# Kernel optimization log

Measured on AMD Instinct MI355X. Metric: run time of the kernel, lower is better.

Reference implementation:

```python
import jax, jax.numpy as jnp
import numpy as np

B, C, N, INPUT_DIM = 16, 19, 64, 200
VQ_DIM = 64
NUM_EMBED = 8192
FREQ = INPUT_DIM // 2 + 1  # 101 rfft bins


def setup_inputs() -> dict:
    key = jax.random.key(0)
    k_x, k_pa, k_pp, k_ca, k_cp = jax.random.split(key, 5)
    x = jax.random.normal(k_x, (B, C, N, INPUT_DIM), dtype=jnp.float32)
    # xavier_normal for [FREQ, VQ_DIM]
    std = float(np.sqrt(2.0 / (FREQ + VQ_DIM)))
    proj_amp = jax.random.normal(k_pa, (FREQ, VQ_DIM), dtype=jnp.float32) * std
    proj_phase = jax.random.normal(k_pp, (FREQ, VQ_DIM), dtype=jnp.float32) * std
    codebook_amp = jax.random.uniform(k_ca, (NUM_EMBED, VQ_DIM), dtype=jnp.float32)
    codebook_phase = jax.random.uniform(k_cp, (NUM_EMBED, VQ_DIM), dtype=jnp.float32)
    return {"x": x, "proj_amp": proj_amp, "proj_phase": proj_phase,
            "codebook_amp": codebook_amp, "codebook_phase": codebook_phase}


def _l2norm(v):
    return v / jnp.linalg.norm(v, axis=-1, keepdims=True)


def reference(x, proj_amp, proj_phase, codebook_amp, codebook_phase):
    # rfft over last dim with ortho norm -> [B,C,N,FREQ] complex
    x_fft = jnp.fft.rfft(x, axis=-1, norm="ortho")
    amp = jnp.abs(x_fft)
    phase = jnp.angle(x_fft)
    # project to vq space and L2-normalize features and codebooks
    feat_amp = _l2norm(amp @ proj_amp)        # [B,C,N,D]
    feat_phase = _l2norm(phase @ proj_phase)  # [B,C,N,D]
    cb_amp = _l2norm(codebook_amp)            # [M,D]
    cb_phase = _l2norm(codebook_phase)        # [M,D]
    # cosine similarity vs codebook, argmax over codebook axis
    sim_amp = jnp.einsum("bcnd,md->bcnm", feat_amp, cb_amp)
    sim_phase = jnp.einsum("bcnd,md->bcnm", feat_phase, cb_phase)
    idx_amp = jnp.argmax(sim_amp, axis=-1)
    idx_phase = jnp.argmax(sim_phase, axis=-1)
    return idx_amp, idx_phase
```

## Files before the change

kernel.cpp:

```cpp
#include <hip/hip_runtime.h>
#include <math.h>

constexpr int ROWS  = 19456;
constexpr int IN_DIM = 200;
constexpr int FREQ  = 101;
constexpr int VQD   = 64;
constexpr int NEMB  = 8192;
constexpr int DFT_BLOCKS = ROWS / 8;

typedef __attribute__((ext_vector_type(8))) short short8;
typedef __attribute__((ext_vector_type(4))) float floatx4;

__device__ __forceinline__ unsigned short f2bf(float v) {
    unsigned int u = __builtin_bit_cast(unsigned int, v);
    unsigned int r = u + 0x7fffu + ((u >> 16) & 1u);
    return (unsigned short)(r >> 16);
}
__device__ __forceinline__ float bf2f(unsigned short b) {
    unsigned int u = ((unsigned int)b) << 16;
    return __builtin_bit_cast(float, u);
}

__device__ __forceinline__ void cis_exact(int r, double& c, double& s) {
    if (r == 0)        { c =  1.0; s =  0.0; }
    else if (r == 50)  { c =  0.0; s = -1.0; }
    else if (r == 100) { c = -1.0; s =  0.0; }
    else if (r == 150) { c =  0.0; s =  1.0; }
    else {
        double ang = -6.283185307179586476925286766559 * (double)r / (double)IN_DIM;
        c = cos(ang); s = sin(ang);
    }
}

#define GLOAD_LDS(gp, lp) __builtin_amdgcn_global_load_lds( \
    (const __attribute__((address_space(1))) unsigned int*)(gp), \
    (__attribute__((address_space(3))) unsigned int*)(lp), 16, 0, 0)

constexpr size_t align256(size_t x) { return (x + 255) & ~(size_t)255; }
constexpr size_t SZ_FB    = (size_t)2 * ROWS * VQD * sizeof(unsigned short);
constexpr size_t OFF_FTH  = 0;
constexpr size_t OFF_FTL  = align256(OFF_FTH + SZ_FB);
constexpr size_t SZ_CBB   = (size_t)2 * NEMB * VQD * sizeof(unsigned short);
constexpr size_t OFF_CBH  = align256(OFF_FTL + SZ_FB);
constexpr size_t OFF_CBL  = align256(OFF_CBH + SZ_CBB);
constexpr size_t SZ_FD    = (size_t)2 * ROWS * VQD * sizeof(double);
constexpr size_t OFF_FD   = align256(OFF_CBL + SZ_CBB);
constexpr size_t SZ_INV   = (size_t)2 * NEMB * sizeof(double);
constexpr size_t OFF_INV  = align256(OFF_FD + SZ_FD);
constexpr size_t SZ_PI    = (size_t)2 * 4 * ROWS * sizeof(int);
constexpr size_t OFF_PI1  = align256(OFF_INV + SZ_INV);
constexpr size_t OFF_PI2  = align256(OFF_PI1 + SZ_PI);

__global__ __launch_bounds__(256) void dft_cb_kernel(
    const float* __restrict__ x, const float* __restrict__ projA, const float* __restrict__ projP,
    const float* __restrict__ cbA, const float* __restrict__ cbP,
    unsigned short* __restrict__ ftH, unsigned short* __restrict__ ftL, double* __restrict__ featD,
    unsigned short* __restrict__ cbH, unsigned short* __restrict__ cbL, double* __restrict__ invnD)
{
    __shared__ __align__(16) char smem[32128];
    const int tid = threadIdx.x;

    if (blockIdx.x >= DFT_BLOCKS) {
        float* tile = (float*)smem;
        float* inv  = (float*)(smem + 16640);
        const int bid2 = blockIdx.x - DFT_BLOCKS;
        const int which = bid2 >> 7;
        const int m0 = (bid2 & 127) * 64;
        const float* cb = which ? cbP : cbA;
        for (int e = tid; e < 4096; e += 256) {
            int c = e >> 6, d = e & 63;
            tile[c * 65 + d] = cb[(size_t)(m0 + c) * VQD + d];
        }
        __syncthreads();
        if (tid < 64) {
            double s = 0.0;
            for (int d2 = 0; d2 < 64; ++d2) { double v = (double)tile[tid * 65 + d2]; s += v * v; }
            inv[tid] = (float)(1.0 / sqrt(s));
            invnD[(size_t)which * NEMB + m0 + tid] = 1.0 / sqrt(s);
        }
        __syncthreads();
        for (int e = tid; e < 4096; e += 256) {
            int c = e >> 6, d = e & 63;
            float v = tile[c * 65 + d] * inv[c];
            unsigned short hb = f2bf(v);
            unsigned short lb = f2bf(v - bf2f(hb));
            size_t o = ((size_t)which * NEMB + m0 + c) * VQD + d;
            cbH[o] = hb; cbL[o] = lb;
        }
        return;
    }

    float*  xsT  = (float*)smem;
    double* xpD  = (double*)(smem + 6400);
    double* xmD  = (double*)(smem + 12800);
    double* reS  = (double*)(smem + 19200);
    double* imS  = (double*)(smem + 25664);
    double* reT  = (double*)smem;
    double* imT  = (double*)(smem + 6464);
    double* accS = (double*)smem;
    const int r0 = blockIdx.x * 8;

    for (int e = tid; e < 8 * IN_DIM; e += 256) {
        int r = e / IN_DIM, n = e - r * IN_DIM;
        xsT[n * 8 + r] = x[(size_t)(r0 + r) * IN_DIM + n];
    }
    __syncthreads();

    for (int e = tid; e < 99 * 8; e += 256) {
        int n = (e >> 3) + 1, r = e & 7;
        double a = (double)xsT[n * 8 + r];
        double b = (double)xsT[(IN_DIM - n) * 8 + r];
        xpD[n * 8 + r] = a + b;
        xmD[n * 8 + r] = a - b;
    }
    __syncthreads();

    const int k = tid & 127, half = tid >> 7;
    double re[8], im[8];
    if (k < FREQ) {
        double c1, s1;
        cis_exact(k, c1, s1);
        const int n0 = half ? 51 : 1;
        double wc, ws;
        cis_exact((int)(((long long)k * n0) % IN_DIM), wc, ws);
#pragma unroll
        for (int r = 0; r < 8; ++r) { re[r] = 0.0; im[r] = 0.0; }
        if (half) {
            double sg = (k & 1) ? -1.0 : 1.0;
#pragma unroll
            for (int r = 0; r < 8; ++r)
                re[r] = (double)xsT[r] + sg * (double)xsT[100 * 8 + r];
        }
        const int nEnd = half ? 100 : 51;
        for (int n = n0; n < nEnd; ++n) {
            const double* xpn = xpD + n * 8;
            const double* xmn = xmD + n * 8;
#pragma unroll
            for (int r = 0; r < 8; ++r) {
                re[r] = fma(xpn[r], wc, re[r]);
                im[r] = fma(xmn[r], ws, im[r]);
            }
            double nwc = wc * c1 - ws * s1;
            double nws = wc * s1 + ws * c1;
            wc = nwc; ws = nws;
        }
        if (half) {
#pragma unroll
            for (int r = 0; r < 8; ++r) { reS[k * 8 + r] = re[r]; imS[k * 8 + r] = im[r]; }
        }
    }
    __syncthreads();
    if (half == 0 && k < FREQ) {
#pragma unroll
        for (int r = 0; r < 8; ++r) { re[r] += reS[k * 8 + r]; im[r] += imS[k * 8 + r]; }
#pragma unroll
        for (int r = 0; r < 8; ++r) { reT[k * 8 + r] = re[r]; imT[k * 8 + r] = im[r]; }
    }
    __syncthreads();
    for (int e = tid; e < FREQ * 8; e += 256) {
        double c = reT[e], sn = imT[e];
        reS[e] = sqrt(c * c + sn * sn);
        imS[e] = atan2(sn, c);
    }
    __syncthreads();

    const int d = tid & 63, which = (tid >> 6) & 1, grp = tid >> 7;
    const float*  proj = which ? projP : projA;
    const double* src  = which ? imS : reS;
    double acc[8];
#pragma unroll
    for (int r = 0; r < 8; ++r) acc[r] = 0.0;
    const int kkA = grp ? 51 : 0;
    const int kkB = grp ? FREQ : 51;
    for (int kk = kkA; kk < kkB; ++kk) {
        double p = (double)proj[kk * VQD + d];
#pragma unroll
        for (int r = 0; r < 8; ++r) acc[r] += src[kk * 8 + r] * p;
    }
    if (grp) {
#pragma unroll
        for (int r = 0; r < 8; ++r) accS[(tid & 127) * 8 + r] = acc[r];
    }
    __syncthreads();
    if (grp == 0) {
#pragma unroll
        for (int r = 0; r < 8; ++r) acc[r] += accS[tid * 8 + r];
#pragma unroll
        for (int r = 0; r < 8; ++r) {
            size_t rowi = (size_t)which * ROWS + r0 + r;
            float vf = (float)acc[r];
            unsigned short hb = f2bf(vf);
            unsigned short lb = f2bf(vf - bf2f(hb));
            ftH[rowi * VQD + d] = hb;
            ftL[rowi * VQD + d] = lb;
            featD[rowi * VQD + d] = acc[r];
        }
    }
}

#define MFMA(a, b, c) __builtin_amdgcn_mfma_f32_16x16x32_bf16(a, b, c, 0, 0, 0)
#define UPD(val, s) do { float _v = (val); \
    bool _c1 = _v > b1v[s]; bool _c2 = _v > b2v[s]; \
    b2v[s] = _c1 ? b1v[s] : (_c2 ? _v : b2v[s]); \
    b2i[s] = _c1 ? b1i[s] : (_c2 ? idx : b2i[s]); \
    b1v[s] = _c1 ? _v : b1v[s]; \
    b1i[s] = _c1 ? idx : b1i[s]; } while (0)

__global__ __launch_bounds__(256, 3) void argmax_kernel(
    const unsigned short* __restrict__ ftH, const unsigned short* __restrict__ ftL,
    const unsigned short* __restrict__ cbH, const unsigned short* __restrict__ cbL,
    int* __restrict__ pi1, int* __restrict__ pi2)
{
    __shared__ __align__(16) char lds[33792];
    const int tid = threadIdx.x;
    const int f = blockIdx.y, z = blockIdx.z;
    const int r0 = blockIdx.x * 128;
    const int w = tid >> 6, lane = tid & 63;
    const int q = lane >> 4, cl = lane & 15;

    const unsigned short* ftHb = ftH + (size_t)f * ROWS * VQD;
    const unsigned short* ftLb = ftL + (size_t)f * ROWS * VQD;
    const unsigned short* cbHb = cbH + (size_t)f * NEMB * VQD;
    const unsigned short* cbLb = cbL + (size_t)f * NEMB * VQD;

    short8 aH00, aH01, aH10, aH11, aL00, aL01, aL10, aL11;
    {
        const size_t baseA = (size_t)(r0 + w * 32 + cl) * VQD + q * 8;
        const size_t baseB = baseA + (size_t)16 * VQD;
        aH00 = *(const short8*)(ftHb + baseA);
        aH01 = *(const short8*)(ftHb + baseA + 32);
        aH10 = *(const short8*)(ftHb + baseB);
        aH11 = *(const short8*)(ftHb + baseB + 32);
        aL00 = *(const short8*)(ftLb + baseA);
        aL01 = *(const short8*)(ftLb + baseA + 32);
        aL10 = *(const short8*)(ftLb + baseB);
        aL11 = *(const short8*)(ftLb + baseB + 32);
    }

    float b1v[8], b2v[8]; int b1i[8], b2i[8];
#pragma unroll
    for (int s = 0; s < 8; ++s) { b1v[s] = -INFINITY; b2v[s] = -INFINITY; b1i[s] = 0; b2i[s] = 0; }

    const int cBase = tid >> 3;
    const int jel   = (((tid & 7) ^ (cBase & 7)) << 3);
    const unsigned short* gH = cbHb + (size_t)(z * 2048 + cBase) * VQD + jel;
    const unsigned short* gL = cbLb + (size_t)(z * 2048 + cBase) * VQD + jel;

    const int p0 = ((q ^ (cl & 7)) << 4);
    const int p1 = p0 ^ 64;

#pragma unroll
    for (int r = 0; r < 2; ++r) {
        const size_t gofs = (size_t)(32 * r) * VQD;
        GLOAD_LDS(gH + gofs, lds + w * 1024 + r * 4096);
        GLOAD_LDS(gL + gofs, lds + 8192 + w * 1024 + r * 4096);
    }

    for (int it = 0; it < 32; ++it) {
        __syncthreads();
        if (it < 31) {
            char* nbuf = lds + ((it + 1) & 1) * 16384;
            const size_t gbase = (size_t)((it + 1) * 64) * VQD;
#pragma unroll
            for (int r = 0; r < 2; ++r) {
                const size_t gofs = gbase + (size_t)(32 * r) * VQD;
                GLOAD_LDS(gH + gofs, nbuf + w * 1024 + r * 4096);
                GLOAD_LDS(gL + gofs, nbuf + 8192 + w * 1024 + r * 4096);
            }
        }

        const char* buf = lds + (it & 1) * 16384;
        const int cbase = z * 2048 + it * 64;
#pragma unroll
        for (int nt = 0; nt < 4; ++nt) {
            const char* row = buf + (nt * 16 + cl) * 128;
            short8 bH0 = *(const short8*)(row + p0);
            short8 bH1 = *(const short8*)(row + p1);
            short8 bL0 = *(const short8*)(row + 8192 + p0);
            short8 bL1 = *(const short8*)(row + 8192 + p1);

            floatx4 acc0 = {0.f, 0.f, 0.f, 0.f};
            floatx4 acc1 = {0.f, 0.f, 0.f, 0.f};
            acc0 = MFMA(aH00, bH0, acc0);  acc1 = MFMA(aH10, bH0, acc1);
            acc0 = MFMA(aH01, bH1, acc0);  acc1 = MFMA(aH11, bH1, acc1);
            acc0 = MFMA(aH00, bL0, acc0);  acc1 = MFMA(aH10, bL0, acc1);
            acc0 = MFMA(aH01, bL1, acc0);  acc1 = MFMA(aH11, bL1, acc1);
            acc0 = MFMA(aL00, bH0, acc0);  acc1 = MFMA(aL10, bH0, acc1);
            acc0 = MFMA(aL01, bH1, acc0);  acc1 = MFMA(aL11, bH1, acc1);

            const int idx = cbase + nt * 16 + cl;
#pragma unroll
            for (int i = 0; i < 4; ++i) { UPD(acc0[i], i); UPD(acc1[i], 4 + i); }
        }
    }

    __syncthreads();
    float* redv = (float*)lds;
    int*   redi = (int*)(lds + 128 * 33 * 4);
#pragma unroll
    for (int s = 0; s < 8; ++s) {
        int rowl = w * 32 + ((s & 4) << 2) + q * 4 + (s & 3);
        int base = rowl * 33 + cl * 2;
        redv[base]     = b1v[s]; redi[base]     = b1i[s];
        redv[base + 1] = b2v[s]; redi[base + 1] = b2i[s];
    }
    __syncthreads();
    if (tid < 128) {
        float v1 = -INFINITY, v2 = -INFINITY; int i1 = 0x7fffffff, i2 = 0x7fffffff;
        for (int e = 0; e < 32; ++e) {
            float v = redv[tid * 33 + e]; int id = redi[tid * 33 + e];
            if (v > v1 || (v == v1 && id < i1)) { v2 = v1; i2 = i1; v1 = v; i1 = id; }
            else if (v > v2 || (v == v2 && id < i2)) { v2 = v; i2 = id; }
        }
        size_t p = ((size_t)(f * 4 + z)) * ROWS + r0 + tid;
        pi1[p] = i1; pi2[p] = i2;
    }
}

__global__ __launch_bounds__(256) void rescore_kernel(
    const double* __restrict__ featD, const double* __restrict__ invnD,
    const float* __restrict__ cbA, const float* __restrict__ cbP,
    const int* __restrict__ pi1, const int* __restrict__ pi2,
    int* __restrict__ out)
{
    const int tid = threadIdx.x;
    const int lane = tid & 63, wave = tid >> 6;
    const int task = blockIdx.x * 4 + wave;
    const int f = task / ROWS;
    const int row = task - f * ROWS;
    const float* cb = f ? cbP : cbA;
    const double fd = featD[((size_t)f * ROWS + row) * VQD + lane];

    int idxs[8];
#pragma unroll
    for (int c = 0; c < 8; ++c) {
        int zz = c >> 1;
        size_t p = ((size_t)(f * 4 + zz)) * ROWS + row;
        idxs[c] = (c & 1) ? pi2[p] : pi1[p];
    }
    double cv[8];
#pragma unroll
    for (int c = 0; c < 8; ++c)
        cv[c] = (double)cb[(size_t)idxs[c] * VQD + lane];

    double bestv = -1.0e300; int besti = 0x7fffffff;
#pragma unroll
    for (int c = 0; c < 8; ++c) {
        double t = fd * cv[c];
        for (int m = 32; m >= 1; m >>= 1) t += __shfl_xor(t, m, 64);
        double sim = t * invnD[(size_t)f * NEMB + idxs[c]];
        int idx = idxs[c];
        if (sim > bestv || (sim == bestv && idx < besti)) { bestv = sim; besti = idx; }
    }
    if (lane == 0) out[task] = besti;
}

extern "C" void kernel_launch(void* const* d_in, const int* in_sizes, int n_in,
                              void* d_out, int out_size, void* d_ws, size_t ws_size,
                              hipStream_t stream)
{
    const float* x     = (const float*)d_in[0];
    const float* projA = (const float*)d_in[1];
    const float* projP = (const float*)d_in[2];
    const float* cbA   = (const float*)d_in[3];
    const float* cbP   = (const float*)d_in[4];

    char* ws = (char*)d_ws;
    unsigned short* ftH   = (unsigned short*)(ws + OFF_FTH);
    unsigned short* ftL   = (unsigned short*)(ws + OFF_FTL);
    unsigned short* cbHp  = (unsigned short*)(ws + OFF_CBH);
    unsigned short* cbLp  = (unsigned short*)(ws + OFF_CBL);
    double*         featD = (double*)(ws + OFF_FD);
    double*         invnD = (double*)(ws + OFF_INV);
    int*            pi1   = (int*)(ws + OFF_PI1);
    int*            pi2   = (int*)(ws + OFF_PI2);

    dft_cb_kernel<<<DFT_BLOCKS + 256, 256, 0, stream>>>(
        x, projA, projP, cbA, cbP, ftH, ftL, featD, cbHp, cbLp, invnD);
    argmax_kernel<<<dim3(ROWS / 128, 2, 4), 256, 0, stream>>>(ftH, ftL, cbHp, cbLp, pi1, pi2);
    rescore_kernel<<<(2 * ROWS) / 4, 256, 0, stream>>>(featD, invnD, cbA, cbP, pi1, pi2, (int*)d_out);
}
```

Before: 316.6 us.

## Compute DFT and projection in fp32 with fp64 fallback for small-magnitude bins

Switches the DFT accumulation, amplitude/phase computation and the frequency-to-VQ projection from double to float, shrinking shared memory and using faster fp32 FMAs. Bins whose squared magnitude is small are recomputed exactly in double precision, so the phase from atan2 stays accurate where fp32 rounding would flip it. The twiddle recurrence stays in double. The change trades some accuracy in the features, and in the downstream argmax, for cheaper arithmetic, and the fallback path adds divergent per-element loops.

```diff
diff --git a/kernel.cpp b/kernel.cpp
--- a/kernel.cpp
+++ b/kernel.cpp
@@ -57,7 +57,7 @@
     unsigned short* __restrict__ ftH, unsigned short* __restrict__ ftL, double* __restrict__ featD,
     unsigned short* __restrict__ cbH, unsigned short* __restrict__ cbL, double* __restrict__ invnD)
 {
-    __shared__ __align__(16) char smem[32128];
+    __shared__ __align__(16) char smem[20064];
     const int tid = threadIdx.x;
 
     if (blockIdx.x >= DFT_BLOCKS) {
@@ -90,33 +90,31 @@
         return;
     }
 
-    float*  xsT  = (float*)smem;
-    double* xpD  = (double*)(smem + 6400);
-    double* xmD  = (double*)(smem + 12800);
-    double* reS  = (double*)(smem + 19200);
-    double* imS  = (double*)(smem + 25664);
-    double* reT  = (double*)smem;
-    double* imT  = (double*)(smem + 6464);
-    double* accS = (double*)smem;
+    float* xsT  = (float*)smem;
+    float* xpS  = (float*)(smem + 7200);
+    float* xmS  = (float*)(smem + 10400);
+    float* reS  = (float*)(smem + 13600);
+    float* imS  = (float*)(smem + 16832);
+    float* accS = (float*)(smem + 7200);
     const int r0 = blockIdx.x * 8;
 
     for (int e = tid; e < 8 * IN_DIM; e += 256) {
         int r = e / IN_DIM, n = e - r * IN_DIM;
-        xsT[n * 8 + r] = x[(size_t)(r0 + r) * IN_DIM + n];
+        xsT[n * 9 + r] = x[(size_t)(r0 + r) * IN_DIM + n];
     }
     __syncthreads();
 
     for (int e = tid; e < 99 * 8; e += 256) {
         int n = (e >> 3) + 1, r = e & 7;
-        double a = (double)xsT[n * 8 + r];
-        double b = (double)xsT[(IN_DIM - n) * 8 + r];
-        xpD[n * 8 + r] = a + b;
-        xmD[n * 8 + r] = a - b;
+        float a = xsT[n * 9 + r];
+        float b = xsT[(IN_DIM - n) * 9 + r];
+        xpS[n * 8 + r] = a + b;
+        xmS[n * 8 + r] = a - b;
     }
     __syncthreads();
 
     const int k = tid & 127, half = tid >> 7;
-    double re[8], im[8];
+    float re[8], im[8];
     if (k < FREQ) {
         double c1, s1;
         cis_exact(k, c1, s1);
@@ -124,24 +122,25 @@
         double wc, ws;
         cis_exact((int)(((long long)k * n0) % IN_DIM), wc, ws);
 #pragma unroll
-        for (int r = 0; r < 8; ++r) { re[r] = 0.0; im[r] = 0.0; }
+        for (int r = 0; r < 8; ++r) { re[r] = 0.f; im[r] = 0.f; }
         if (half) {
-            double sg = (k & 1) ? -1.0 : 1.0;
+            float sg = (k & 1) ? -1.f : 1.f;
 #pragma unroll
             for (int r = 0; r < 8; ++r)
-                re[r] = (double)xsT[r] + sg * (double)xsT[100 * 8 + r];
+                re[r] = xsT[r] + sg * xsT[100 * 9 + r];
         }
         const int nEnd = half ? 100 : 51;
         for (int n = n0; n < nEnd; ++n) {
-            const double* xpn = xpD + n * 8;
-            const double* xmn = xmD + n * 8;
+            const float* xpn = xpS + n * 8;
+            const float* xmn = xmS + n * 8;
+            float wcf = (float)wc, wsf = (float)ws;
 #pragma unroll
             for (int r = 0; r < 8; ++r) {
-                re[r] = fma(xpn[r], wc, re[r]);
-                im[r] = fma(xmn[r], ws, im[r]);
+                re[r] = fmaf(xpn[r], wcf, re[r]);
+                im[r] = fmaf(xmn[r], wsf, im[r]);
             }
-            double nwc = wc * c1 - ws * s1;
-            double nws = wc * s1 + ws * c1;
+            double nwc = fma(wc, c1, -ws * s1);
+            double nws = fma(wc, s1,  ws * c1);
             wc = nwc; ws = nws;
         }
         if (half) {
@@ -152,30 +151,55 @@
     __syncthreads();
     if (half == 0 && k < FREQ) {
 #pragma unroll
-        for (int r = 0; r < 8; ++r) { re[r] += reS[k * 8 + r]; im[r] += imS[k * 8 + r]; }
-#pragma unroll
-        for (int r = 0; r < 8; ++r) { reT[k * 8 + r] = re[r]; imT[k * 8 + r] = im[r]; }
+        for (int r = 0; r < 8; ++r) {
+            re[r] += reS[k * 8 + r]; im[r] += imS[k * 8 + r];
+            reS[k * 8 + r] = re[r];  imS[k * 8 + r] = im[r];
+        }
     }
     __syncthreads();
     for (int e = tid; e < FREQ * 8; e += 256) {
-        double c = reT[e], sn = imT[e];
-        reS[e] = sqrt(c * c + sn * sn);
-        imS[e] = atan2(sn, c);
+        float c = reS[e], s = imS[e];
+        float a2 = fmaf(c, c, s * s);
+        float ampv, phv;
+        if (a2 >= 0.04f) {
+            ampv = sqrtf(a2);
+            phv  = atan2f(s, c);
+        } else {
+            const int kk = e >> 3, rr = e & 7;
+            double sg = (kk & 1) ? -1.0 : 1.0;
+            double reD = (double)xsT[rr] + sg * (double)xsT[100 * 9 + rr];
+            double imD = 0.0;
+            double c1, s1;
+            cis_exact(kk, c1, s1);
+            double wc = c1, ws = s1;
+            for (int n = 1; n < 100; ++n) {
+                double a = (double)xsT[n * 9 + rr];
+                double b = (double)xsT[(IN_DIM - n) * 9 + rr];
+                reD = fma(a + b, wc, reD);
+                imD = fma(a - b, ws, imD);
+                double nwc = fma(wc, c1, -ws * s1);
+                double nws = fma(wc, s1,  ws * c1);
+                wc = nwc; ws = nws;
+            }
+            ampv = (float)sqrt(reD * reD + imD * imD);
+            phv  = (float)atan2(imD, reD);
+        }
+        reS[e] = ampv; imS[e] = phv;
     }
     __syncthreads();
 
     const int d = tid & 63, which = (tid >> 6) & 1, grp = tid >> 7;
-    const float*  proj = which ? projP : projA;
-    const double* src  = which ? imS : reS;
-    double acc[8];
-#pragma unroll
-    for (int r = 0; r < 8; ++r) acc[r] = 0.0;
+    const float* proj = which ? projP : projA;
+    const float* srcF = which ? imS : reS;
+    float acc[8];
+#pragma unroll
+    for (int r = 0; r < 8; ++r) acc[r] = 0.f;
     const int kkA = grp ? 51 : 0;
     const int kkB = grp ? FREQ : 51;
     for (int kk = kkA; kk < kkB; ++kk) {
-        double p = (double)proj[kk * VQD + d];
-#pragma unroll
-        for (int r = 0; r < 8; ++r) acc[r] += src[kk * 8 + r] * p;
+        float p = proj[kk * VQD + d];
+#pragma unroll
+        for (int r = 0; r < 8; ++r) acc[r] = fmaf(srcF[kk * 8 + r], p, acc[r]);
     }
     if (grp) {
 #pragma unroll
@@ -188,12 +212,12 @@
 #pragma unroll
         for (int r = 0; r < 8; ++r) {
             size_t rowi = (size_t)which * ROWS + r0 + r;
-            float vf = (float)acc[r];
+            float vf = acc[r];
             unsigned short hb = f2bf(vf);
             unsigned short lb = f2bf(vf - bf2f(hb));
             ftH[rowi * VQD + d] = hb;
             ftL[rowi * VQD + d] = lb;
-            featD[rowi * VQD + d] = acc[r];
+            featD[rowi * VQD + d] = (double)acc[r];
         }
     }
 }
```

New measurement: 306.1 us. 1.03x faster.
